# Kernel optimization log

Hardware: AMD Instinct MI355X
Metric: run time of the kernel (lower is better)

## Reference

```python
import jax, jax.numpy as jnp
import numpy as np

N_NODES = 100000
N_EDGES = 1600000
NUM_GRAPHS = 4096
EPS = 1e-5


def _glorot(key, shape):
    fan_in, fan_out = shape[0], shape[1]
    lim = float(np.sqrt(6.0 / (fan_in + fan_out)))
    return jax.random.uniform(key, shape, jnp.float32, -lim, lim)


def setup_inputs() -> dict:
    key = jax.random.key(0)
    ks = jax.random.split(key, 32)
    inp = {}
    inp['x'] = jax.random.normal(ks[0], (N_NODES, 32), jnp.float32)
    inp['edge_attr'] = jax.random.uniform(ks[1], (N_EDGES, 8), jnp.float32)
    inp['edge_index'] = jax.random.randint(ks[2], (2, N_EDGES), 0, N_NODES, jnp.int32)
    inp['batch'] = jnp.sort(jax.random.randint(ks[3], (N_NODES,), 0, NUM_GRAPHS, jnp.int32))
    inp['num_graphs'] = NUM_GRAPHS
    # node/edge embeddings
    inp['Wn'] = _glorot(ks[4], (32, 64)); inp['bn_'] = jnp.zeros((64,), jnp.float32)
    inp['We'] = _glorot(ks[5], (8, 16)); inp['be_'] = jnp.zeros((16,), jnp.float32)
    # conv1: 2*64+16=144 -> 128 -> 64
    inp['W1a'] = _glorot(ks[6], (144, 128)); inp['b1a'] = jnp.zeros((128,), jnp.float32)
    inp['W1b'] = _glorot(ks[7], (128, 64)); inp['b1b'] = jnp.zeros((64,), jnp.float32)
    # conv2: 2*64+16=144 -> 64 -> 32
    inp['W2a'] = _glorot(ks[8], (144, 64)); inp['b2a'] = jnp.zeros((64,), jnp.float32)
    inp['W2b'] = _glorot(ks[9], (64, 32)); inp['b2b'] = jnp.zeros((32,), jnp.float32)
    # conv3: 2*32+16=80 -> 32 -> 16
    inp['W3a'] = _glorot(ks[10], (80, 32)); inp['b3a'] = jnp.zeros((32,), jnp.float32)
    inp['W3b'] = _glorot(ks[11], (32, 16)); inp['b3b'] = jnp.zeros((16,), jnp.float32)
    # batchnorm affine params
    inp['g1'] = jnp.ones((64,), jnp.float32); inp['beta1'] = jnp.zeros((64,), jnp.float32)
    inp['g2'] = jnp.ones((32,), jnp.float32); inp['beta2'] = jnp.zeros((32,), jnp.float32)
    inp['g3'] = jnp.ones((16,), jnp.float32); inp['beta3'] = jnp.zeros((16,), jnp.float32)
    # final fc 16 -> 12
    inp['Wfc'] = _glorot(ks[12], (16, 12)); inp['bfc'] = jnp.zeros((12,), jnp.float32)
    return inp


def _conv(x, e_emb, src, dst, Wa, ba, Wb, bb, n_nodes):
    # PyG: x_i = x[target]=x[dst], x_j = x[source]=x[src]; message MLP; mean-aggregate at dst
    m = jnp.concatenate([x[dst], x[src], e_emb], axis=1)      # [E, 2*in+edge]
    m = jax.nn.relu(m @ Wa + ba) @ Wb + bb                    # [E, out]
    s = jax.ops.segment_sum(m, dst, num_segments=n_nodes)
    cnt = jax.ops.segment_sum(jnp.ones((m.shape[0], 1), m.dtype), dst, num_segments=n_nodes)
    return s / jnp.maximum(cnt, 1.0)


def _batchnorm(x, g, b):
    mu = jnp.mean(x, axis=0)
    var = jnp.mean(jnp.square(x - mu), axis=0)
    return (x - mu) * jax.lax.rsqrt(var + EPS) * g + b


def reference(x, edge_attr, edge_index, batch, num_graphs,
              Wn, bn_, We, be_, W1a, b1a, W1b, b1b, W2a, b2a, W2b, b2b,
              W3a, b3a, W3b, b3b, g1, beta1, g2, beta2, g3, beta3, Wfc, bfc):
    n_nodes = x.shape[0]
    src, dst = edge_index[0], edge_index[1]
    e_emb = jax.nn.relu(edge_attr @ We + be_)                 # [E, 16]
    h = jax.nn.relu(x @ Wn + bn_)                             # [N, 64]
    h = _conv(h, e_emb, src, dst, W1a, b1a, W1b, b1b, n_nodes)
    h = jax.nn.relu(_batchnorm(h, g1, beta1))
    h = _conv(h, e_emb, src, dst, W2a, b2a, W2b, b2b, n_nodes)
    h = jax.nn.relu(_batchnorm(h, g2, beta2))
    h = _conv(h, e_emb, src, dst, W3a, b3a, W3b, b3b, n_nodes)
    h = jax.nn.relu(_batchnorm(h, g3, beta3))
    # global mean pool per graph
    s = jax.ops.segment_sum(h, batch, num_segments=num_graphs)
    cnt = jax.ops.segment_sum(jnp.ones((n_nodes, 1), h.dtype), batch, num_segments=num_graphs)
    pooled = s / jnp.maximum(cnt, 1.0)                        # [G, 16]
    return jax.nn.sigmoid(pooled @ Wfc + bfc)                 # [G, 12]
```

## Files before the change

kernel.cpp:

```cpp
#include <hip/hip_runtime.h>
#include <hip/hip_bf16.h>
#include <cstdio>


#define N_NODES 100000
#define N_EDGES 1600000
#define NUM_GRAPHS 4096
#define BK_SH 9
#define NBK ((N_NODES + 511) >> 9)
#define CHUNK 4096

typedef unsigned short u16;
typedef unsigned int u32;
typedef _Float16 h2 __attribute__((ext_vector_type(2)));

#if defined(__has_builtin)
#if __has_builtin(__builtin_amdgcn_fdot2)
#define DOT2(a, b, c) __builtin_amdgcn_fdot2((a), (b), (c), false)
#endif
#endif
#ifndef DOT2
#define DOT2(a, b, c) ((c) + (float)(a).x * (float)(b).x + (float)(a).y * (float)(b).y)
#endif

__device__ __forceinline__ float b2f(u16 u) { union { u32 i; float f; } c; c.i = ((u32)u) << 16; return c.f; }
__device__ __forceinline__ float b2f_lo(u32 u) { union { u32 i; float f; } c; c.i = u << 16; return c.f; }
__device__ __forceinline__ float b2f_hi(u32 u) { union { u32 i; float f; } c; c.i = u & 0xffff0000u; return c.f; }
__device__ __forceinline__ u16 f2b(float f) {
    __hip_bfloat16 h = __float2bfloat16(f);
    return *reinterpret_cast<u16*>(&h);
}

template <int CPL>
__device__ __forceinline__ void ld_bf16(const u16* base, float out[CPL]) {
    if constexpr (CPL == 1) {
        out[0] = b2f(*base);
    } else {
        u32 v = *(const u32*)base;
        out[0] = b2f_lo(v); out[1] = b2f_hi(v);
    }
}
template <int CPL>
__device__ __forceinline__ void ld_f32(const float* base, float out[CPL]) {
    if constexpr (CPL == 1) {
        out[0] = *base;
    } else {
        float2 v = *(const float2*)base;
        out[0] = v.x; out[1] = v.y;
    }
}

__global__ __launch_bounds__(256) void hist_k(const int* __restrict__ dst, int* __restrict__ hist) {
    int e = blockIdx.x * 256 + threadIdx.x;
    if (e < N_EDGES) atomicAdd(&hist[dst[e]], 1);
}

__global__ __launch_bounds__(256) void scan_part_k(const int* __restrict__ hist,
        int* __restrict__ excl, int* __restrict__ bsum) {
    __shared__ int sm[256];
    int t = threadIdx.x, b = blockIdx.x;
    int base = b * 1024 + t * 4;
    int v0 = (base + 0 < N_NODES) ? hist[base + 0] : 0;
    int v1 = (base + 1 < N_NODES) ? hist[base + 1] : 0;
    int v2 = (base + 2 < N_NODES) ? hist[base + 2] : 0;
    int v3 = (base + 3 < N_NODES) ? hist[base + 3] : 0;
    int tsum = v0 + v1 + v2 + v3;
    sm[t] = tsum;
    __syncthreads();
    for (int o = 1; o < 256; o <<= 1) {
        int x = (t >= o) ? sm[t - o] : 0;
        __syncthreads();
        sm[t] += x;
        __syncthreads();
    }
    int texcl = sm[t] - tsum;
    if (base + 0 < N_NODES) excl[base + 0] = texcl;
    if (base + 1 < N_NODES) excl[base + 1] = texcl + v0;
    if (base + 2 < N_NODES) excl[base + 2] = texcl + v0 + v1;
    if (base + 3 < N_NODES) excl[base + 3] = texcl + v0 + v1 + v2;
    if (t == 255) bsum[b] = sm[255];
}

__global__ __launch_bounds__(256) void scan_top_k(int* __restrict__ bsum, int* __restrict__ boff,
        int nb, int* __restrict__ row_ptr_last) {
    __shared__ int sm[256];
    int t = threadIdx.x;
    int v = (t < nb) ? bsum[t] : 0;
    sm[t] = v;
    __syncthreads();
    for (int o = 1; o < 256; o <<= 1) {
        int x = (t >= o) ? sm[t - o] : 0;
        __syncthreads();
        sm[t] += x;
        __syncthreads();
    }
    if (t < nb) boff[t] = sm[t] - v;
    if (t == 0) *row_ptr_last = sm[255];
}

__global__ __launch_bounds__(256) void scan_add_k(int* __restrict__ excl, const int* __restrict__ boff,
        int* __restrict__ row_ptr) {
    int i = blockIdx.x * 256 + threadIdx.x;
    if (i >= N_NODES) return;
    row_ptr[i] = excl[i] + boff[i >> 10];
}

__global__ __launch_bounds__(256) void bucketcur_k(const int* __restrict__ row_ptr, int* __restrict__ bcur) {
    int b = blockIdx.x * 256 + threadIdx.x;
    if (b < NBK) bcur[b] = row_ptr[b << BK_SH];
}

__global__ __launch_bounds__(256) void route_k(const int* __restrict__ src, const int* __restrict__ dst,
        int* __restrict__ bcur, int2* __restrict__ tmp) {
    __shared__ int hcnt[NBK];
    __shared__ int hbase[NBK];
    const int t = threadIdx.x;
    const int e0 = blockIdx.x * CHUNK;
    const int e1 = (e0 + CHUNK < N_EDGES) ? e0 + CHUNK : N_EDGES;
    for (int i = t; i < NBK; i += 256) hcnt[i] = 0;
    __syncthreads();
    for (int e = e0 + t; e < e1; e += 256)
        atomicAdd(&hcnt[dst[e] >> BK_SH], 1);
    __syncthreads();
    for (int i = t; i < NBK; i += 256) {
        int c = hcnt[i];
        hbase[i] = (c > 0) ? atomicAdd(&bcur[i], c) : 0;
        hcnt[i] = 0;
    }
    __syncthreads();
    for (int e = e0 + t; e < e1; e += 256) {
        int d = dst[e];
        int b = d >> BK_SH;
        int r = atomicAdd(&hcnt[b], 1);
        int2 q;
        q.x = src[e];
        q.y = e | ((d & 511) << 21);
        tmp[hbase[b] + r] = q;
    }
}

__global__ __launch_bounds__(256) void fine_k(const int* __restrict__ row_ptr,
        const int2* __restrict__ tmp, int2* __restrict__ epk) {
    __shared__ int cur[512];
    const int t = threadIdx.x;
    const int b = blockIdx.x;
    const int n0 = b << BK_SH;
    for (int i = t; i < 512; i += 256) {
        int n = n0 + i;
        cur[i] = row_ptr[(n < N_NODES) ? n : N_NODES];
    }
    __syncthreads();
    const int nEnd = (n0 + 512 < N_NODES) ? n0 + 512 : N_NODES;
    const int p0 = row_ptr[n0], p1 = row_ptr[nEnd];
    for (int i = p0 + t; i < p1; i += 256) {
        int2 q = tmp[i];
        int dl = (q.y >> 21) & 511;
        int pos = atomicAdd(&cur[dl], 1);
        int2 o;
        o.x = q.x;
        o.y = q.y & 0x1FFFFF;
        epk[pos] = o;
    }
}

__global__ __launch_bounds__(256) void ubound_k(const int* __restrict__ row_ptr, int* __restrict__ sn) {
    int u = blockIdx.x * 256 + threadIdx.x;
    if (u > 25000) return;
    if (u == 25000) { sn[u] = N_NODES; return; }
    int target = u * 64;
    int lo = 0, hi = N_NODES;
    while (lo < hi) {
        int mid = (lo + hi) >> 1;
        if (row_ptr[mid] >= target) hi = mid; else lo = mid + 1;
    }
    sn[u] = lo;
}

__global__ __launch_bounds__(256) void edge_emb_k(const float* __restrict__ ea,
        const float* __restrict__ We, const float* __restrict__ be,
        const int2* __restrict__ epk, _Float16* __restrict__ e16s) {
    int idx = blockIdx.x * 256 + threadIdx.x;
    int p = idx >> 4, k = idx & 15;
    int e = epk[p].y;
    float4 a0 = *(const float4*)(ea + (size_t)e * 8);
    float4 a1 = *(const float4*)(ea + (size_t)e * 8 + 4);
    float acc = be[k];
    acc += a0.x * We[0 * 16 + k];
    acc += a0.y * We[1 * 16 + k];
    acc += a0.z * We[2 * 16 + k];
    acc += a0.w * We[3 * 16 + k];
    acc += a1.x * We[4 * 16 + k];
    acc += a1.y * We[5 * 16 + k];
    acc += a1.z * We[6 * 16 + k];
    acc += a1.w * We[7 * 16 + k];
    e16s[(size_t)idx] = (_Float16)fmaxf(acc, 0.f);
}

__global__ __launch_bounds__(256) void node_emb2_k(const float* __restrict__ x,
        const float* __restrict__ Wn, const float* __restrict__ bn_, float* __restrict__ h) {
    constexpr int C = 64, F = 32, TILE = 64;
    __shared__ float xs[TILE * F];
    const int t = threadIdx.x;
    const int grp = t / C;
    const int c = t % C;
    float w[F];
#pragma unroll
    for (int k = 0; k < F; ++k) w[k] = Wn[(size_t)k * 64 + c];
    const float bias = bn_[c];
    const float4* xsrc = (const float4*)x;
    float4* xs4 = (float4*)xs;

    for (int v0 = blockIdx.x * TILE; v0 < N_NODES; v0 += gridDim.x * TILE) {
        __syncthreads();
        for (int i = t; i < TILE * F / 4; i += 256) {
            int vv = v0 + (i * 4) / F;
            float4 val;
            if (vv < N_NODES) val = xsrc[(size_t)v0 * (F / 4) + i];
            else { val.x = val.y = val.z = val.w = 0.f; }
            xs4[i] = val;
        }
        __syncthreads();
        const int base = grp * 16;
        const int nmax = (N_NODES - v0 - base >= 16) ? 16
                        : (N_NODES - v0 - base > 0 ? N_NODES - v0 - base : 0);
        for (int n = 0; n < nmax; ++n) {
            const int v = v0 + base + n;
            const float4* xr4 = (const float4*)&xs[(base + n) * F];
            float a0 = bias, a1 = 0.f, a2 = 0.f, a3 = 0.f;
#pragma unroll
            for (int k4 = 0; k4 < F / 4; ++k4) {
                float4 hv = xr4[k4];
                a0 += hv.x * w[4 * k4 + 0];
                a1 += hv.y * w[4 * k4 + 1];
                a2 += hv.z * w[4 * k4 + 2];
                a3 += hv.w * w[4 * k4 + 3];
            }
            h[(size_t)v * 64 + c] = fmaxf((a0 + a1) + (a2 + a3), 0.f);
        }
    }
}

template <int F, int H, bool BN>
__global__ __launch_bounds__(256) void proj_k(const float* __restrict__ h,
        const float* __restrict__ Wa, const float* __restrict__ ba,
        const float* __restrict__ stats, const float* __restrict__ g, const float* __restrict__ beta,
        float* __restrict__ Pd, u16* __restrict__ Ps) {
    constexpr int C2 = 2 * H;
    constexpr int NPB = 256 / C2;
    constexpr int TILE = 16 * NPB;
    __shared__ float hs[TILE][F];
    __shared__ float sc[BN ? F : 1];
    __shared__ float shv[BN ? F : 1];
    const int t = threadIdx.x;
    if constexpr (BN) {
        if (t < F) {
            const float invN = 1.0f / (float)N_NODES;
            float mu = stats[t] * invN;
            float ex2 = stats[F + t] * invN;
            float var = fmaxf(ex2 - mu * mu, 0.f);
            float rs = rsqrtf(var + 1e-5f);
            float scale = rs * g[t];
            sc[t] = scale;
            shv[t] = beta[t] - mu * scale;
        }
    }
    const int grp = t / C2;
    const int c = t % C2;
    const bool is_src = (c >= H);
    const int cc = is_src ? (c - H) : c;
    float w[F];
    const float* wcol = Wa + (size_t)(is_src ? F : 0) * H + cc;
#pragma unroll
    for (int k = 0; k < F; ++k) w[k] = wcol[(size_t)k * H];
    const float bias = is_src ? 0.f : ba[cc];

    for (int v0 = blockIdx.x * TILE; v0 < N_NODES; v0 += gridDim.x * TILE) {
        __syncthreads();
        for (int i = t; i < TILE * F; i += 256) {
            int vv = v0 + i / F;
            float val = (vv < N_NODES) ? h[(size_t)vv * F + (i % F)] : 0.f;
            if constexpr (BN) val = fmaxf(val * sc[i % F] + shv[i % F], 0.f);
            hs[i / F][i % F] = val;
        }
        __syncthreads();
        const int base = grp * 16;
        const int nmax = (N_NODES - v0 - base >= 16) ? 16
                        : (N_NODES - v0 - base > 0 ? N_NODES - v0 - base : 0);
#pragma unroll 2
        for (int n = 0; n < nmax; ++n) {
            const int v = v0 + base + n;
            const float4* hr4 = (const float4*)hs[base + n];
            float a0 = bias, a1 = 0.f, a2 = 0.f, a3 = 0.f;
#pragma unroll
            for (int k4 = 0; k4 < F / 4; ++k4) {
                float4 hv = hr4[k4];
                a0 += hv.x * w[4 * k4 + 0];
                a1 += hv.y * w[4 * k4 + 1];
                a2 += hv.z * w[4 * k4 + 2];
                a3 += hv.w * w[4 * k4 + 3];
            }
            float acc = (a0 + a1) + (a2 + a3);
            if (is_src) Ps[(size_t)v * H + cc] = f2b(acc);
            else        Pd[(size_t)v * H + cc] = acc;
        }
    }
}

template <int H>
__global__ __launch_bounds__(256) void conv_k(
        const int* __restrict__ sn, const int* __restrict__ row_ptr,
        const int2* __restrict__ epk, const _Float16* __restrict__ e16s,
        float* __restrict__ Pd, const u16* __restrict__ Ps,
        const float* __restrict__ Wae) {
    constexpr int SL = (H >= 64) ? 64 : 32;
    constexpr int NPW = 64 / SL;
    constexpr int CPL = H / SL;
    const int wave = threadIdx.x >> 6, lane = threadIdx.x & 63;
    const int sub = lane / SL;
    const int sl = lane % SL;
    const int c0 = sl * CPL;
    h2 w2h[8][CPL];
#pragma unroll
    for (int k2 = 0; k2 < 8; ++k2)
#pragma unroll
        for (int j = 0; j < CPL; ++j) {
            h2 t;
            t.x = (_Float16)Wae[(2 * k2) * H + c0 + j];
            t.y = (_Float16)Wae[(2 * k2 + 1) * H + c0 + j];
            w2h[k2][j] = t;
        }

    const int uid = (blockIdx.x * 4 + wave) * NPW + sub;
    const int vbeg = sn[uid], vend = sn[uid + 1];

    for (int v = vbeg; v < vend; ++v) {
        const int vv = (SL == 64) ? __builtin_amdgcn_readfirstlane(v) : v;
        float pd[CPL], acc[CPL];
        ld_f32<CPL>(&Pd[(size_t)vv * H + c0], pd);
#pragma unroll
        for (int j = 0; j < CPL; ++j) acc[j] = 0.f;
        const int p0 = row_ptr[vv], p1 = row_ptr[vv + 1];
        const int deg = p1 - p0;

        auto edge = [&](uint4 ra, uint4 rb, const float ps[CPL]) {
            union { u32 u; h2 h; } cv;
            h2 ev[8];
            cv.u = ra.x; ev[0] = cv.h; cv.u = ra.y; ev[1] = cv.h;
            cv.u = ra.z; ev[2] = cv.h; cv.u = ra.w; ev[3] = cv.h;
            cv.u = rb.x; ev[4] = cv.h; cv.u = rb.y; ev[5] = cv.h;
            cv.u = rb.z; ev[6] = cv.h; cv.u = rb.w; ev[7] = cv.h;
            float z[CPL];
#pragma unroll
            for (int j = 0; j < CPL; ++j) z[j] = pd[j] + ps[j];
#pragma unroll
            for (int k2 = 0; k2 < 8; ++k2)
#pragma unroll
                for (int j = 0; j < CPL; ++j) z[j] = DOT2(ev[k2], w2h[k2][j], z[j]);
#pragma unroll
            for (int j = 0; j < CPL; ++j) acc[j] += fmaxf(z[j], 0.f);
        };

        int p = p0;
        for (; p + 3 < p1; p += 4) {
            int2 q0 = epk[p], q1 = epk[p + 1], q2 = epk[p + 2], q3 = epk[p + 3];
            const uint4* e0 = (const uint4*)(e16s + (size_t)p * 16);
            uint4 a0 = e0[0], a1 = e0[1];
            uint4 b0 = e0[2], b1 = e0[3];
            uint4 g0 = e0[4], g1 = e0[5];
            uint4 d0 = e0[6], d1 = e0[7];
            float ps0[CPL], ps1[CPL], ps2[CPL], ps3[CPL];
            ld_bf16<CPL>(&Ps[(size_t)q0.x * H + c0], ps0);
            ld_bf16<CPL>(&Ps[(size_t)q1.x * H + c0], ps1);
            ld_bf16<CPL>(&Ps[(size_t)q2.x * H + c0], ps2);
            ld_bf16<CPL>(&Ps[(size_t)q3.x * H + c0], ps3);
            edge(a0, a1, ps0);
            edge(b0, b1, ps1);
            edge(g0, g1, ps2);
            edge(d0, d1, ps3);
        }
        for (; p < p1; ++p) {
            int2 q0 = epk[p];
            const uint4* e0 = (const uint4*)(e16s + (size_t)p * 16);
            uint4 a0 = e0[0], a1 = e0[1];
            float ps0[CPL];
            ld_bf16<CPL>(&Ps[(size_t)q0.x * H + c0], ps0);
            edge(a0, a1, ps0);
        }

        const float invd = (deg > 0) ? 1.f / (float)deg : 0.f;
        if constexpr (CPL == 2) {
            float2 o; o.x = acc[0] * invd; o.y = acc[1] * invd;
            *(float2*)&Pd[(size_t)vv * H + c0] = o;
        } else {
            Pd[(size_t)vv * H + c0] = acc[0] * invd;
        }
    }
}

template <int H, int Fo>
__global__ __launch_bounds__(256) void matvec2_k(const float* __restrict__ m,
        const int* __restrict__ row_ptr,
        const float* __restrict__ Wb, const float* __restrict__ bb,
        float* __restrict__ y, float* __restrict__ stats) {
    constexpr int FoC = (Fo < 32) ? Fo : 32;
    constexpr int CG = Fo / FoC;
    constexpr int NPW = 32 / FoC;
    constexpr int NG = 4 / CG;
    constexpr int SLOTS = NG * NPW;
    constexpr int KH = H / 2;
    constexpr int TILE = 4096 / H;
    constexpr int J = TILE / SLOTS;

    __shared__ float hs[TILE * H];
    __shared__ int ptile[TILE + 1];
    __shared__ float sh[2 * Fo];

    const int t = threadIdx.x;
    const int wave = t >> 6, lane = t & 63;
    const int kh = lane >> 5;
    const int r = lane & 31;
    const int c_lo = r % FoC;
    const int s = r / FoC;
    const int cg = wave % CG;
    const int ng = wave / CG;
    const int c = cg * FoC + c_lo;
    const int slot = ng * NPW + s;

    for (int i = t; i < 2 * Fo; i += 256) sh[i] = 0.f;

    float w[KH];
#pragma unroll
    for (int k = 0; k < KH; ++k) w[k] = Wb[(size_t)(kh * KH + k) * Fo + c];
    const float bias = bb[c];
    float s1 = 0.f, s2 = 0.f;

    const float4* msrc = (const float4*)m;
    float4* hs4 = (float4*)hs;

    for (int v0 = blockIdx.x * TILE; v0 < N_NODES; v0 += gridDim.x * TILE) {
        __syncthreads();
#pragma unroll
        for (int q = t; q < 1024; q += 256) {
            int node = (q * 4) / H;
            float4 val;
            if (v0 + node < N_NODES) val = msrc[(size_t)v0 * (H / 4) + q];
            else { val.x = val.y = val.z = val.w = 0.f; }
            hs4[q] = val;
        }
        for (int i = t; i <= TILE; i += 256) {
            int v = v0 + i;
            ptile[i] = row_ptr[v < N_NODES ? v : N_NODES];
        }
        __syncthreads();

        for (int j = 0; j < J; ++j) {
            const int n = slot + j * SLOTS;
            const int v = v0 + n;
            const float4* hr4 = (const float4*)&hs[n * H + kh * KH];
            float a0 = 0.f, a1 = 0.f, a2 = 0.f, a3 = 0.f;
#pragma unroll
            for (int k4 = 0; k4 < KH / 4; ++k4) {
                float4 hv = hr4[k4];
                a0 += hv.x * w[4 * k4 + 0];
                a1 += hv.y * w[4 * k4 + 1];
                a2 += hv.z * w[4 * k4 + 2];
                a3 += hv.w * w[4 * k4 + 3];
            }
            float half = (a0 + a1) + (a2 + a3);
            float total = half + __shfl_xor(half, 32) + bias;
            if (kh == 0 && v < N_NODES) {
                const int deg = ptile[n + 1] - ptile[n];
                float val = (deg > 0) ? total : 0.f;
                y[(size_t)v * Fo + c] = val;
                s1 += val; s2 += val * val;
            }
        }
    }

    __syncthreads();
    if (kh == 0) {
        atomicAdd(&sh[c], s1);
        atomicAdd(&sh[Fo + c], s2);
    }
    __syncthreads();
    if (t < 2 * Fo) atomicAdd(&stats[t], sh[t]);
}

__global__ __launch_bounds__(256) void pool_bn_k(const float* __restrict__ y,
        const float* __restrict__ stats, const float* __restrict__ g, const float* __restrict__ beta,
        const int* __restrict__ batch, float* __restrict__ pool, int* __restrict__ gcnt) {
    int idx = blockIdx.x * 256 + threadIdx.x;
    if (idx >= N_NODES * 16) return;
    int v = idx >> 4, c = idx & 15;
    const float invN = 1.0f / (float)N_NODES;
    float mu = stats[c] * invN;
    float ex2 = stats[16 + c] * invN;
    float var = fmaxf(ex2 - mu * mu, 0.f);
    float rs = rsqrtf(var + 1e-5f);
    float val = fmaxf((y[idx] - mu) * rs * g[c] + beta[c], 0.f);
    int b = batch[v];
    atomicAdd(&pool[b * 16 + c], val);
    if (c == 0) atomicAdd(&gcnt[b], 1);
}

__global__ __launch_bounds__(256) void out_k(const float* __restrict__ pool,
        const int* __restrict__ gcnt, const float* __restrict__ Wfc,
        const float* __restrict__ bfc, float* __restrict__ out) {
    int idx = blockIdx.x * 256 + threadIdx.x;
    if (idx >= NUM_GRAPHS * 12) return;
    int g = idx / 12, o = idx % 12;
    int cnt = gcnt[g];
    float inv = 1.0f / (float)(cnt > 0 ? cnt : 1);
    float acc = bfc[o];
#pragma unroll
    for (int k = 0; k < 16; ++k) acc += pool[g * 16 + k] * inv * Wfc[k * 12 + o];
    out[idx] = 1.0f / (1.0f + expf(-acc));
}

extern "C" void kernel_launch(void* const* d_in, const int* in_sizes, int n_in,
                              void* d_out, int out_size, void* d_ws, size_t ws_size,
                              hipStream_t stream) {
    const size_t N = N_NODES, E = N_EDGES, G = NUM_GRAPHS;
    const float* x = (const float*)d_in[0];
    const float* ea = (const float*)d_in[1];
    const int* ei = (const int*)d_in[2];
    const int* srcv = ei;
    const int* dstv = ei + E;
    const int* batch = (const int*)d_in[3];
    const float* Wn = (const float*)d_in[5];  const float* bn_ = (const float*)d_in[6];
    const float* We = (const float*)d_in[7];  const float* be_ = (const float*)d_in[8];
    const float* W1a = (const float*)d_in[9]; const float* b1a = (const float*)d_in[10];
    const float* W1b = (const float*)d_in[11]; const float* b1b = (const float*)d_in[12];
    const float* W2a = (const float*)d_in[13]; const float* b2a = (const float*)d_in[14];
    const float* W2b = (const float*)d_in[15]; const float* b2b = (const float*)d_in[16];
    const float* W3a = (const float*)d_in[17]; const float* b3a = (const float*)d_in[18];
    const float* W3b = (const float*)d_in[19]; const float* b3b = (const float*)d_in[20];
    const float* g1 = (const float*)d_in[21]; const float* be1 = (const float*)d_in[22];
    const float* g2 = (const float*)d_in[23]; const float* be2 = (const float*)d_in[24];
    const float* g3 = (const float*)d_in[25]; const float* be3 = (const float*)d_in[26];
    const float* Wfc = (const float*)d_in[27]; const float* bfc = (const float*)d_in[28];

    char* base = (char*)d_ws;
    size_t off = 0;
    auto take = [&](size_t bytes) { size_t o = off; off += (bytes + 255) & ~(size_t)255; return o; };
    int* hist = (int*)(base + take(N * 4));
    int* excl = (int*)(base + take(N * 4));
    int* row_ptr = (int*)(base + take((N + 1) * 4));
    int* bsum = (int*)(base + take(256 * 4));
    int* boff = (int*)(base + take(256 * 4));
    int* bcur = (int*)(base + take(256 * 4));
    int* sn = (int*)(base + take(25001 * 4));
    int2* epk = (int2*)(base + take(E * 8));
    int2* tmp = (int2*)(base + take(E * 8));
    float* hbuf = (float*)(base + take(N * 64 * 4));
    float* Pd = (float*)(base + take(N * 128 * 4));
    u16* Ps = (u16*)(base + take(N * 128 * 2));
    _Float16* e16s = (_Float16*)(base + take(E * 16 * 2));
    float* stats = (float*)(base + take(256 * 4));
    float* pool = (float*)(base + take(G * 16 * 4));
    int* gcnt = (int*)(base + take(G * 4));
    if (off > ws_size) {
        fprintf(stderr, "kernel_launch: ws too small: need %zu have %zu\n", off, ws_size);
        return;
    }

    const int NB = (N_NODES + 1023) / 1024;

    hipMemsetAsync(hist, 0, N * 4, stream);
    hist_k<<<dim3((E + 255) / 256), dim3(256), 0, stream>>>(dstv, hist);
    scan_part_k<<<dim3(NB), dim3(256), 0, stream>>>(hist, excl, bsum);
    scan_top_k<<<dim3(1), dim3(256), 0, stream>>>(bsum, boff, NB, &row_ptr[N_NODES]);
    scan_add_k<<<dim3((N + 255) / 256), dim3(256), 0, stream>>>(excl, boff, row_ptr);
    bucketcur_k<<<dim3(1), dim3(256), 0, stream>>>(row_ptr, bcur);
    route_k<<<dim3((N_EDGES + CHUNK - 1) / CHUNK), dim3(256), 0, stream>>>(srcv, dstv, bcur, tmp);
    fine_k<<<dim3(NBK), dim3(256), 0, stream>>>(row_ptr, tmp, epk);
    ubound_k<<<dim3((25001 + 255) / 256), dim3(256), 0, stream>>>(row_ptr, sn);

    edge_emb_k<<<dim3(E * 16 / 256), dim3(256), 0, stream>>>(ea, We, be_, epk, e16s);
    node_emb2_k<<<dim3(1563), dim3(256), 0, stream>>>(x, Wn, bn_, hbuf);

    proj_k<64, 128, false><<<dim3(6250), dim3(256), 0, stream>>>(hbuf, W1a, b1a, nullptr, nullptr, nullptr, Pd, Ps);
    conv_k<128><<<dim3(6250), dim3(256), 0, stream>>>(sn, row_ptr, epk, e16s, Pd, Ps, W1a + 128 * 128);
    hipMemsetAsync(stats, 0, 256 * 4, stream);
    matvec2_k<128, 64><<<dim3(1024), dim3(256), 0, stream>>>(Pd, row_ptr, W1b, b1b, hbuf, stats);

    proj_k<64, 64, true><<<dim3(3125), dim3(256), 0, stream>>>(hbuf, W2a, b2a, stats, g1, be1, Pd, Ps);
    conv_k<64><<<dim3(6250), dim3(256), 0, stream>>>(sn, row_ptr, epk, e16s, Pd, Ps, W2a + 128 * 64);
    hipMemsetAsync(stats, 0, 256 * 4, stream);
    matvec2_k<64, 32><<<dim3(1024), dim3(256), 0, stream>>>(Pd, row_ptr, W2b, b2b, hbuf, stats);

    proj_k<32, 32, true><<<dim3(1563), dim3(256), 0, stream>>>(hbuf, W3a, b3a, stats, g2, be2, Pd, Ps);
    conv_k<32><<<dim3(3125), dim3(256), 0, stream>>>(sn, row_ptr, epk, e16s, Pd, Ps, W3a + 64 * 32);
    hipMemsetAsync(stats, 0, 256 * 4, stream);
    matvec2_k<32, 16><<<dim3(1024), dim3(256), 0, stream>>>(Pd, row_ptr, W3b, b3b, hbuf, stats);

    hipMemsetAsync(pool, 0, G * 16 * 4, stream);
    hipMemsetAsync(gcnt, 0, G * 4, stream);
    pool_bn_k<<<dim3((N * 16 + 255) / 256), dim3(256), 0, stream>>>(hbuf, stats, g3, be3, batch, pool, gcnt);
    out_k<<<dim3((G * 12 + 255) / 256), dim3(256), 0, stream>>>(pool, gcnt, Wfc, bfc, (float*)d_out);
}
```

Measured before the change: 942.7 us.

## Compute per-edge embedding projection with MFMA in conv kernels

Replaces the per-lane fdot2 loop that multiplies each edge's 16-wide fp16 embedding by the edge-weight slice with a 16x16x32 fp16 MFMA. Each wave handles one node and processes its edges in groups of 16 rows, with K zero-padded from 16 to 32. Results are gathered per row alongside the bf16 source projections and then reduced across the four lane groups with shuffles. Each wave now handles exactly one unit, so the H=32 launch doubles its grid. The risk is wasted MFMA work on low-degree nodes and the half-empty K dimension, plus scattered Ps loads and extra shuffles.

```diff
diff --git a/kernel.cpp b/kernel.cpp
--- a/kernel.cpp
+++ b/kernel.cpp
@@ -13,41 +13,13 @@
 typedef unsigned short u16;
 typedef unsigned int u32;
 typedef _Float16 h2 __attribute__((ext_vector_type(2)));
-
-#if defined(__has_builtin)
-#if __has_builtin(__builtin_amdgcn_fdot2)
-#define DOT2(a, b, c) __builtin_amdgcn_fdot2((a), (b), (c), false)
-#endif
-#endif
-#ifndef DOT2
-#define DOT2(a, b, c) ((c) + (float)(a).x * (float)(b).x + (float)(a).y * (float)(b).y)
-#endif
+typedef _Float16 f16x8 __attribute__((ext_vector_type(8)));
+typedef float f32x4 __attribute__((ext_vector_type(4)));
 
 __device__ __forceinline__ float b2f(u16 u) { union { u32 i; float f; } c; c.i = ((u32)u) << 16; return c.f; }
-__device__ __forceinline__ float b2f_lo(u32 u) { union { u32 i; float f; } c; c.i = u << 16; return c.f; }
-__device__ __forceinline__ float b2f_hi(u32 u) { union { u32 i; float f; } c; c.i = u & 0xffff0000u; return c.f; }
 __device__ __forceinline__ u16 f2b(float f) {
     __hip_bfloat16 h = __float2bfloat16(f);
     return *reinterpret_cast<u16*>(&h);
-}
-
-template <int CPL>
-__device__ __forceinline__ void ld_bf16(const u16* base, float out[CPL]) {
-    if constexpr (CPL == 1) {
-        out[0] = b2f(*base);
-    } else {
-        u32 v = *(const u32*)base;
-        out[0] = b2f_lo(v); out[1] = b2f_hi(v);
-    }
-}
-template <int CPL>
-__device__ __forceinline__ void ld_f32(const float* base, float out[CPL]) {
-    if constexpr (CPL == 1) {
-        out[0] = *base;
-    } else {
-        float2 v = *(const float2*)base;
-        out[0] = v.x; out[1] = v.y;
-    }
 }
 
 __global__ __launch_bounds__(256) void hist_k(const int* __restrict__ dst, int* __restrict__ hist) {
@@ -307,92 +279,83 @@
 }
 
 template <int H>
-__global__ __launch_bounds__(256) void conv_k(
+__global__ __launch_bounds__(256) void conv_mfma_k(
         const int* __restrict__ sn, const int* __restrict__ row_ptr,
         const int2* __restrict__ epk, const _Float16* __restrict__ e16s,
         float* __restrict__ Pd, const u16* __restrict__ Ps,
         const float* __restrict__ Wae) {
-    constexpr int SL = (H >= 64) ? 64 : 32;
-    constexpr int NPW = 64 / SL;
-    constexpr int CPL = H / SL;
+    constexpr int T = H / 16;
     const int wave = threadIdx.x >> 6, lane = threadIdx.x & 63;
-    const int sub = lane / SL;
-    const int sl = lane % SL;
-    const int c0 = sl * CPL;
-    h2 w2h[8][CPL];
-#pragma unroll
-    for (int k2 = 0; k2 < 8; ++k2)
-#pragma unroll
-        for (int j = 0; j < CPL; ++j) {
-            h2 t;
-            t.x = (_Float16)Wae[(2 * k2) * H + c0 + j];
-            t.y = (_Float16)Wae[(2 * k2 + 1) * H + c0 + j];
-            w2h[k2][j] = t;
-        }
-
-    const int uid = (blockIdx.x * 4 + wave) * NPW + sub;
+    const int l15 = lane & 15;
+    const int kb = lane >> 4;
+    const f32x4 zc = {0.f, 0.f, 0.f, 0.f};
+
+    f16x8 Bt[T];
+#pragma unroll
+    for (int t = 0; t < T; ++t) {
+#pragma unroll
+        for (int j = 0; j < 8; ++j) {
+            int k = kb * 8 + j;
+            Bt[t][j] = (k < 16) ? (_Float16)Wae[(size_t)k * H + t * 16 + l15] : (_Float16)0.f;
+        }
+    }
+
+    const int uid = blockIdx.x * 4 + wave;
     const int vbeg = sn[uid], vend = sn[uid + 1];
 
     for (int v = vbeg; v < vend; ++v) {
-        const int vv = (SL == 64) ? __builtin_amdgcn_readfirstlane(v) : v;
-        float pd[CPL], acc[CPL];
-        ld_f32<CPL>(&Pd[(size_t)vv * H + c0], pd);
-#pragma unroll
-        for (int j = 0; j < CPL; ++j) acc[j] = 0.f;
+        const int vv = __builtin_amdgcn_readfirstlane(v);
         const int p0 = row_ptr[vv], p1 = row_ptr[vv + 1];
         const int deg = p1 - p0;
 
-        auto edge = [&](uint4 ra, uint4 rb, const float ps[CPL]) {
-            union { u32 u; h2 h; } cv;
-            h2 ev[8];
-            cv.u = ra.x; ev[0] = cv.h; cv.u = ra.y; ev[1] = cv.h;
-            cv.u = ra.z; ev[2] = cv.h; cv.u = ra.w; ev[3] = cv.h;
-            cv.u = rb.x; ev[4] = cv.h; cv.u = rb.y; ev[5] = cv.h;
-            cv.u = rb.z; ev[6] = cv.h; cv.u = rb.w; ev[7] = cv.h;
-            float z[CPL];
-#pragma unroll
-            for (int j = 0; j < CPL; ++j) z[j] = pd[j] + ps[j];
-#pragma unroll
-            for (int k2 = 0; k2 < 8; ++k2)
-#pragma unroll
-                for (int j = 0; j < CPL; ++j) z[j] = DOT2(ev[k2], w2h[k2][j], z[j]);
-#pragma unroll
-            for (int j = 0; j < CPL; ++j) acc[j] += fmaxf(z[j], 0.f);
-        };
-
-        int p = p0;
-        for (; p + 3 < p1; p += 4) {
-            int2 q0 = epk[p], q1 = epk[p + 1], q2 = epk[p + 2], q3 = epk[p + 3];
-            const uint4* e0 = (const uint4*)(e16s + (size_t)p * 16);
-            uint4 a0 = e0[0], a1 = e0[1];
-            uint4 b0 = e0[2], b1 = e0[3];
-            uint4 g0 = e0[4], g1 = e0[5];
-            uint4 d0 = e0[6], d1 = e0[7];
-            float ps0[CPL], ps1[CPL], ps2[CPL], ps3[CPL];
-            ld_bf16<CPL>(&Ps[(size_t)q0.x * H + c0], ps0);
-            ld_bf16<CPL>(&Ps[(size_t)q1.x * H + c0], ps1);
-            ld_bf16<CPL>(&Ps[(size_t)q2.x * H + c0], ps2);
-            ld_bf16<CPL>(&Ps[(size_t)q3.x * H + c0], ps3);
-            edge(a0, a1, ps0);
-            edge(b0, b1, ps1);
-            edge(g0, g1, ps2);
-            edge(d0, d1, ps3);
-        }
-        for (; p < p1; ++p) {
-            int2 q0 = epk[p];
-            const uint4* e0 = (const uint4*)(e16s + (size_t)p * 16);
-            uint4 a0 = e0[0], a1 = e0[1];
-            float ps0[CPL];
-            ld_bf16<CPL>(&Ps[(size_t)q0.x * H + c0], ps0);
-            edge(a0, a1, ps0);
+        float pd[T], acc[T];
+#pragma unroll
+        for (int t = 0; t < T; ++t) {
+            pd[t] = Pd[(size_t)vv * H + t * 16 + l15];
+            acc[t] = 0.f;
+        }
+
+        for (int g = p0; g < p1; g += 16) {
+            const int nr = (p1 - g < 16) ? (p1 - g) : 16;
+
+            f16x8 a;
+#pragma unroll
+            for (int j = 0; j < 8; ++j) a[j] = (_Float16)0.f;
+            if (kb < 2 && l15 < nr) {
+                union { uint4 u; f16x8 h; } cv;
+                cv.u = *(const uint4*)(e16s + ((size_t)(g + l15) * 16 + kb * 8));
+                a = cv.h;
+            }
+
+            int s0 = 0, s1 = 0, s2 = 0, s3 = 0;
+            {
+                int R = kb * 4;
+                if (R + 0 < nr) s0 = epk[g + R + 0].x;
+                if (R + 1 < nr) s1 = epk[g + R + 1].x;
+                if (R + 2 < nr) s2 = epk[g + R + 2].x;
+                if (R + 3 < nr) s3 = epk[g + R + 3].x;
+            }
+
+#pragma unroll
+            for (int t = 0; t < T; ++t) {
+                f32x4 D = __builtin_amdgcn_mfma_f32_16x16x32_f16(a, Bt[t], zc, 0, 0, 0);
+                const int R = kb * 4;
+                const int cofs = t * 16 + l15;
+                if (R + 0 < nr) acc[t] += fmaxf(D[0] + pd[t] + b2f(Ps[(size_t)s0 * H + cofs]), 0.f);
+                if (R + 1 < nr) acc[t] += fmaxf(D[1] + pd[t] + b2f(Ps[(size_t)s1 * H + cofs]), 0.f);
+                if (R + 2 < nr) acc[t] += fmaxf(D[2] + pd[t] + b2f(Ps[(size_t)s2 * H + cofs]), 0.f);
+                if (R + 3 < nr) acc[t] += fmaxf(D[3] + pd[t] + b2f(Ps[(size_t)s3 * H + cofs]), 0.f);
+            }
         }
 
         const float invd = (deg > 0) ? 1.f / (float)deg : 0.f;
-        if constexpr (CPL == 2) {
-            float2 o; o.x = acc[0] * invd; o.y = acc[1] * invd;
-            *(float2*)&Pd[(size_t)vv * H + c0] = o;
-        } else {
-            Pd[(size_t)vv * H + c0] = acc[0] * invd;
+#pragma unroll
+        for (int t = 0; t < T; ++t) {
+            float tot = acc[t];
+            tot += __shfl_xor(tot, 16);
+            tot += __shfl_xor(tot, 32);
+            if (kb == (t & 3))
+                Pd[(size_t)vv * H + t * 16 + l15] = tot * invd;
         }
     }
 }
@@ -580,17 +543,17 @@
     node_emb2_k<<<dim3(1563), dim3(256), 0, stream>>>(x, Wn, bn_, hbuf);
 
     proj_k<64, 128, false><<<dim3(6250), dim3(256), 0, stream>>>(hbuf, W1a, b1a, nullptr, nullptr, nullptr, Pd, Ps);
-    conv_k<128><<<dim3(6250), dim3(256), 0, stream>>>(sn, row_ptr, epk, e16s, Pd, Ps, W1a + 128 * 128);
+    conv_mfma_k<128><<<dim3(6250), dim3(256), 0, stream>>>(sn, row_ptr, epk, e16s, Pd, Ps, W1a + 128 * 128);
     hipMemsetAsync(stats, 0, 256 * 4, stream);
     matvec2_k<128, 64><<<dim3(1024), dim3(256), 0, stream>>>(Pd, row_ptr, W1b, b1b, hbuf, stats);
 
     proj_k<64, 64, true><<<dim3(3125), dim3(256), 0, stream>>>(hbuf, W2a, b2a, stats, g1, be1, Pd, Ps);
-    conv_k<64><<<dim3(6250), dim3(256), 0, stream>>>(sn, row_ptr, epk, e16s, Pd, Ps, W2a + 128 * 64);
+    conv_mfma_k<64><<<dim3(6250), dim3(256), 0, stream>>>(sn, row_ptr, epk, e16s, Pd, Ps, W2a + 128 * 64);
     hipMemsetAsync(stats, 0, 256 * 4, stream);
     matvec2_k<64, 32><<<dim3(1024), dim3(256), 0, stream>>>(Pd, row_ptr, W2b, b2b, hbuf, stats);
 
     proj_k<32, 32, true><<<dim3(1563), dim3(256), 0, stream>>>(hbuf, W3a, b3a, stats, g2, be2, Pd, Ps);
-    conv_k<32><<<dim3(3125), dim3(256), 0, stream>>>(sn, row_ptr, epk, e16s, Pd, Ps, W3a + 64 * 32);
+    conv_mfma_k<32><<<dim3(6250), dim3(256), 0, stream>>>(sn, row_ptr, epk, e16s, Pd, Ps, W3a + 64 * 32);
     hipMemsetAsync(stats, 0, 256 * 4, stream);
     matvec2_k<32, 16><<<dim3(1024), dim3(256), 0, stream>>>(Pd, row_ptr, W3b, b3b, hbuf, stats);
 
```

After: 1.339 ms. 1.42x slower.
